# Optimization experiments

Measured on AMD Instinct MI355X. Metric: run time of the kernel, lower is better.

The kernel has to match this reference:

```python
import jax, jax.numpy as jnp
import numpy as np
import math

DIM = 2048
N_HEADS = 32
N_KV_HEADS = 8
HEAD_DIM = DIM // N_HEADS  # 64
N_REP = N_HEADS // N_KV_HEADS  # 4
BSZ, SEQ = 2, 2048


def setup_inputs() -> dict:
    key = jax.random.key(0)
    ks = jax.random.split(key, 8)
    x = jax.random.normal(ks[0], (BSZ, SEQ, DIM), dtype=jnp.float32)
    # rotary tables, [seq, head_dim//2]
    inv_freq = 1.0 / (10000.0 ** (np.arange(0, HEAD_DIM, 2, dtype=np.float32) / HEAD_DIM))
    t = np.arange(SEQ, dtype=np.float32)
    freqs = np.outer(t, inv_freq)
    freqs_cos = jnp.asarray(np.cos(freqs))
    freqs_sin = jnp.asarray(np.sin(freqs))
    s = 0.02
    wq = jax.random.normal(ks[1], (DIM, N_HEADS * HEAD_DIM), dtype=jnp.float32) * s
    wk = jax.random.normal(ks[2], (DIM, N_KV_HEADS * HEAD_DIM), dtype=jnp.float32) * s
    wv = jax.random.normal(ks[3], (DIM, N_KV_HEADS * HEAD_DIM), dtype=jnp.float32) * s
    wo = jax.random.normal(ks[4], (N_HEADS * HEAD_DIM, DIM), dtype=jnp.float32) * s
    return {"x": x, "freqs_cos": freqs_cos, "freqs_sin": freqs_sin,
            "wq": wq, "wk": wk, "wv": wv, "wo": wo}


def _apply_rotary(xq, xk, cos, sin):
    # xq: [b,s,h,d], xk: [b,s,kh,d]; cos/sin: [s, d//2]
    def rot(t):
        tr = t[..., 0::2]  # even -> real
        ti = t[..., 1::2]  # odd  -> imag
        c = cos[None, :, None, :]
        s_ = sin[None, :, None, :]
        or_ = tr * c - ti * s_
        oi_ = tr * s_ + ti * c
        # interleave back: [..., d//2, 2] -> [..., d]
        return jnp.stack([or_, oi_], axis=-1).reshape(t.shape)
    return rot(xq), rot(xk)


def reference(x, freqs_cos, freqs_sin, wq, wk, wv, wo):
    b, s, _ = x.shape
    xq = (x @ wq).reshape(b, s, N_HEADS, HEAD_DIM)
    xk = (x @ wk).reshape(b, s, N_KV_HEADS, HEAD_DIM)
    xv = (x @ wv).reshape(b, s, N_KV_HEADS, HEAD_DIM)
    xq, xk = _apply_rotary(xq, xk, freqs_cos, freqs_sin)
    # repeat_kv: [b,s,kh,d] -> [b,s,kh*n_rep,d]
    xk = jnp.repeat(xk, N_REP, axis=2)
    xv = jnp.repeat(xv, N_REP, axis=2)
    # [b,h,s,d]
    q = xq.transpose(0, 2, 1, 3)
    k = xk.transpose(0, 2, 1, 3)
    v = xv.transpose(0, 2, 1, 3)
    scale = 1.0 / math.sqrt(HEAD_DIM)
    scores = jnp.einsum('bhqd,bhkd->bhqk', q, k) * scale
    causal = jnp.tril(jnp.ones((s, s), dtype=bool))
    scores = jnp.where(causal[None, None], scores, jnp.float32(-jnp.inf))
    probs = jax.nn.softmax(scores, axis=-1)
    out = jnp.einsum('bhqk,bhkd->bhqd', probs, v)  # [b,h,s,d]
    out = out.transpose(0, 2, 1, 3).reshape(b, s, N_HEADS * HEAD_DIM)
    return out @ wo
```

## Files before the change

### kernel.cpp

```cpp
#include <hip/hip_runtime.h>
#include <hip/hip_bf16.h>

typedef __attribute__((ext_vector_type(8))) short short8;
typedef __attribute__((ext_vector_type(4))) float f32x4;

__device__ __forceinline__ unsigned short f2bf(float f) {
  union { float f; unsigned u; } v; v.f = f;
  unsigned r = v.u + 0x7FFFu + ((v.u >> 16) & 1u);
  return (unsigned short)(r >> 16);
}
__device__ __forceinline__ float bf2f(unsigned short h) {
  union { unsigned u; float f; } v; v.u = ((unsigned)h) << 16;
  return v.f;
}
__device__ __forceinline__ unsigned pkbf(float a, float b) {
  __hip_bfloat162 h = __float22bfloat162_rn(float2{a, b});
  union { __hip_bfloat162 h; unsigned u; } cv; cv.h = h;
  return cv.u;
}

__global__ void prep(const float* __restrict__ x, const float* __restrict__ wq,
                     const float* __restrict__ wk, const float* __restrict__ wv,
                     const float* __restrict__ wo, unsigned short* __restrict__ xb,
                     unsigned short* __restrict__ wt, unsigned short* __restrict__ wot) {
  const int z = blockIdx.z, tid = threadIdx.x;
  if (z == 0) {
    int id = blockIdx.y * 64 + blockIdx.x;
#pragma unroll
    for (int rep = 0; rep < 2; ++rep) {
      int i = (rep * 4096 + id) * 256 + tid;
      float4 v = ((const float4*)x)[i];
      ushort4 o;
      o.x = f2bf(v.x); o.y = f2bf(v.y); o.z = f2bf(v.z); o.w = f2bf(v.w);
      ((ushort4*)xb)[i] = o;
    }
    return;
  }
  __shared__ float tile[32][33];
  const float* src;
  unsigned short* dst;
  int N;
  if (z == 1) { src = wq; dst = wt; N = 2048; }
  else if (z == 2) { src = wk; dst = wt + 2048ull * 2048; N = 512; }
  else if (z == 3) { src = wv; dst = wt + 2560ull * 2048; N = 512; }
  else { src = wo; dst = wot; N = 2048; }
  const int K = 2048;
  int n0 = blockIdx.x * 32, k0 = blockIdx.y * 32;
  if (n0 >= N) return;
  int xx = tid & 31, yy = tid >> 5;
#pragma unroll
  for (int j = 0; j < 4; ++j) tile[yy + 8 * j][xx] = src[(size_t)(k0 + yy + 8 * j) * N + n0 + xx];
  __syncthreads();
#pragma unroll
  for (int j = 0; j < 4; ++j) dst[(size_t)(n0 + yy + 8 * j) * K + k0 + xx] = f2bf(tile[xx][yy + 8 * j]);
}

template <int MODE>
__global__ __launch_bounds__(256, 2) void gemm_bt64(const unsigned short* __restrict__ A,
                                                    const unsigned short* __restrict__ Bt,
                                                    void* __restrict__ Cv, int K, int ldc,
                                                    unsigned short* __restrict__ vt,
                                                    const float* __restrict__ fcos,
                                                    const float* __restrict__ fsin) {
  __shared__ alignas(16) unsigned short As[128 * 64];
  __shared__ alignas(16) unsigned short Bs[128 * 64];
  const int t = threadIdx.x;
  const int lane = t & 63, w = t >> 6;
  const int l15 = lane & 15, quad = lane >> 4;
  const int bn0 = blockIdx.x * 128, bm0 = blockIdx.y * 128;
  const int wm = (w >> 1) * 64, wn = (w & 1) * 64;
  const unsigned short* Ab = A + (size_t)bm0 * K;
  const unsigned short* Bb = Bt + (size_t)bn0 * K;
  const int asw = l15 & 7;

  f32x4 acc[4][4];
  const f32x4 zf = {0.f, 0.f, 0.f, 0.f};
#pragma unroll
  for (int i = 0; i < 4; ++i)
#pragma unroll
    for (int j = 0; j < 4; ++j) acc[i][j] = zf;

  for (int k0 = 0; k0 < K; k0 += 64) {
    __syncthreads();
#pragma unroll
    for (int r = 0; r < 4; ++r) {
      int e = r * 256 + t;
      int row = e >> 3, cslot = e & 7;
      int cg = cslot ^ (row & 7);
      const unsigned short* ga = Ab + (size_t)row * K + k0 + cg * 8;
      __builtin_amdgcn_global_load_lds((const __attribute__((address_space(1))) void*)ga,
                                       (__attribute__((address_space(3))) void*)(As + e * 8), 16, 0, 0);
      const unsigned short* gb = Bb + (size_t)row * K + k0 + cg * 8;
      __builtin_amdgcn_global_load_lds((const __attribute__((address_space(1))) void*)gb,
                                       (__attribute__((address_space(3))) void*)(Bs + e * 8), 16, 0, 0);
    }
    __syncthreads();
#pragma unroll
    for (int s = 0; s < 2; ++s) {
      short8 af[4], bf[4];
#pragma unroll
      for (int i = 0; i < 4; ++i)
        af[i] = *reinterpret_cast<const short8*>(As + (wm + i * 16 + l15) * 64 + (((s * 4 + quad) ^ asw) * 8));
#pragma unroll
      for (int j = 0; j < 4; ++j)
        bf[j] = *reinterpret_cast<const short8*>(Bs + (wn + j * 16 + l15) * 64 + (((s * 4 + quad) ^ asw) * 8));
      __builtin_amdgcn_s_setprio(1);
#pragma unroll
      for (int i = 0; i < 4; ++i)
#pragma unroll
        for (int j = 0; j < 4; ++j)
          acc[i][j] = __builtin_amdgcn_mfma_f32_16x16x32_bf16(af[i], bf[j], acc[i][j], 0, 0, 0);
      __builtin_amdgcn_s_setprio(0);
    }
  }

  if (MODE == 1 && bn0 >= 2560) {
    const int b = bm0 >> 11;
#pragma unroll
    for (int i = 0; i < 4; ++i) {
      int srow = (bm0 + wm + i * 16 + quad * 4) & 2047;
#pragma unroll
      for (int j = 0; j < 4; ++j) {
        int vcol = bn0 - 2560 + wn + j * 16 + l15;
        int kvh = vcol >> 6, d = vcol & 63;
        uint2 pk = make_uint2(pkbf(acc[i][j][0], acc[i][j][1]), pkbf(acc[i][j][2], acc[i][j][3]));
        *reinterpret_cast<uint2*>(vt + ((size_t)(b * 8 + kvh) * 64 + d) * 2048 + srow) = pk;
      }
    }
  } else if (MODE == 1 && bn0 >= 2048) {
#pragma unroll
    for (int i = 0; i < 4; ++i)
#pragma unroll
      for (int j = 0; j < 4; ++j)
#pragma unroll
        for (int r = 0; r < 4; ++r) {
          int row = bm0 + wm + i * 16 + quad * 4 + r;
          int s = row & 2047;
          int col = bn0 + wn + j * 16 + l15;
          int fi = ((col - 2048) >> 1) & 31;
          float val = acc[i][j][r];
          float par = __shfl_xor(val, 1, 64);
          float c = fcos[s * 32 + fi], sn = fsin[s * 32 + fi];
          float o = (lane & 1) ? (par * sn + val * c) : (val * c - par * sn);
          ((unsigned short*)Cv)[(size_t)row * ldc + col] = f2bf(o);
        }
  } else {
#pragma unroll
    for (int i = 0; i < 4; ++i)
#pragma unroll
      for (int j = 0; j < 4; ++j)
#pragma unroll
        for (int r = 0; r < 4; ++r) {
          size_t row = (size_t)(bm0 + wm + i * 16 + quad * 4 + r);
          size_t col = (size_t)(bn0 + wn + j * 16 + l15);
          if (MODE == 1)
            ((unsigned short*)Cv)[row * ldc + col] = f2bf(acc[i][j][r]);
          else
            ((float*)Cv)[row * ldc + col] = acc[i][j][r];
        }
  }
}

__global__ __launch_bounds__(256, 4) void flash_attn(const unsigned short* __restrict__ qkv,
                                                     const unsigned short* __restrict__ vt,
                                                     const float* __restrict__ fcos,
                                                     const float* __restrict__ fsin,
                                                     unsigned short* __restrict__ out) {
  __shared__ alignas(16) unsigned short Ks[64 * 64];
  __shared__ alignas(16) unsigned short Vs[64 * 64];
  __shared__ alignas(16) unsigned short Ps[128 * 64];
  const int t = threadIdx.x, lane = t & 63, w = t >> 6;
  const int l15 = lane & 15, quad = lane >> 4;
  const int h = blockIdx.y, b = blockIdx.z;
  const int qb = ((int)blockIdx.x ^ (15 * (h >> 4))) & 15;
  const int q0 = qb * 128;
  const int kvh = h >> 2;
  const size_t rowB = (size_t)b * 2048;
  const unsigned short* Qg = qkv + (rowB + q0) * 2560 + h * 64;
  const unsigned short* Kg = qkv + rowB * 2560 + 2048 + kvh * 64;
  const unsigned short* Vtg = vt + (size_t)(b * 8 + kvh) * 64 * 2048;
  const float SC = 0.18033688011112042f;

  short8 qf[2][2];
#pragma unroll
  for (int mt = 0; mt < 2; ++mt)
#pragma unroll
    for (int s = 0; s < 2; ++s) {
      int qrow = w * 32 + mt * 16 + l15;
      short8 raw = *reinterpret_cast<const short8*>(Qg + (size_t)qrow * 2560 + s * 32 + quad * 8);
      f32x4 c4 = *reinterpret_cast<const f32x4*>(fcos + (size_t)(q0 + qrow) * 32 + s * 16 + quad * 4);
      f32x4 s4 = *reinterpret_cast<const f32x4*>(fsin + (size_t)(q0 + qrow) * 32 + s * 16 + quad * 4);
      short8 o;
#pragma unroll
      for (int k = 0; k < 4; ++k) {
        float xr = bf2f((unsigned short)raw[2 * k]);
        float xi = bf2f((unsigned short)raw[2 * k + 1]);
        o[2 * k] = (short)f2bf((xr * c4[k] - xi * s4[k]) * SC);
        o[2 * k + 1] = (short)f2bf((xr * s4[k] + xi * c4[k]) * SC);
      }
      qf[mt][s] = o;
    }

  const f32x4 zf = {0.f, 0.f, 0.f, 0.f};
  f32x4 oacc[2][4], lacc[2];
#pragma unroll
  for (int mt = 0; mt < 2; ++mt) {
    lacc[mt] = zf;
#pragma unroll
    for (int nt = 0; nt < 4; ++nt) oacc[mt][nt] = zf;
  }
  short8 onesf;
#pragma unroll
  for (int k = 0; k < 8; ++k) onesf[k] = (short)0x3F80;

  const int kb_end = 2 * qb + 2;
  const int srow = t >> 3, sc8 = t & 7;
  const int soff = srow * 64 + ((sc8 ^ (srow & 7)) * 8);
  const int asw = l15 & 7;
  short8 kreg[2], vreg[2];
#pragma unroll
  for (int r = 0; r < 2; ++r) {
    kreg[r] = *reinterpret_cast<const short8*>(Kg + (size_t)(srow + 32 * r) * 2560 + sc8 * 8);
    vreg[r] = *reinterpret_cast<const short8*>(Vtg + (size_t)(srow + 32 * r) * 2048 + sc8 * 8);
  }

  for (int kb = 0; kb < kb_end; ++kb) {
    __syncthreads();
#pragma unroll
    for (int r = 0; r < 2; ++r) {
      *reinterpret_cast<short8*>(Ks + soff + r * 32 * 64) = kreg[r];
      *reinterpret_cast<short8*>(Vs + soff + r * 32 * 64) = vreg[r];
    }
    __syncthreads();
    if (kb + 1 < kb_end) {
#pragma unroll
      for (int r = 0; r < 2; ++r) {
        kreg[r] = *reinterpret_cast<const short8*>(Kg + (size_t)((kb + 1) * 64 + srow + 32 * r) * 2560 + sc8 * 8);
        vreg[r] = *reinterpret_cast<const short8*>(Vtg + (size_t)(srow + 32 * r) * 2048 + (kb + 1) * 64 + sc8 * 8);
      }
    }
    const int qmaxw = q0 + w * 32 + 31;
    if (kb * 64 > qmaxw) continue;
    const bool needMask = (kb * 64 + 63) > (q0 + w * 32);

#pragma unroll
    for (int kvt = 0; kvt < 4; ++kvt) {
      f32x4 st0 = zf, st1 = zf;
#pragma unroll
      for (int s = 0; s < 2; ++s) {
        short8 kf = *reinterpret_cast<const short8*>(Ks + (kvt * 16 + l15) * 64 + ((s * 4 + quad) ^ asw) * 8);
        __builtin_amdgcn_s_setprio(1);
        st0 = __builtin_amdgcn_mfma_f32_16x16x32_bf16(kf, qf[0][s], st0, 0, 0, 0);
        st1 = __builtin_amdgcn_mfma_f32_16x16x32_bf16(kf, qf[1][s], st1, 0, 0, 0);
        __builtin_amdgcn_s_setprio(0);
      }
      const int pcol = ((kvt * 2 + (quad >> 1)) ^ asw) * 8 + (quad & 1) * 4;
      if (needMask) {
        const int kvb = kb * 64 + kvt * 16 + quad * 4;
#pragma unroll
        for (int qt = 0; qt < 2; ++qt) {
          const f32x4 stv = qt ? st1 : st0;
          const int qg = q0 + w * 32 + qt * 16 + l15;
          float p[4];
#pragma unroll
          for (int r = 0; r < 4; ++r) {
            float pv = __builtin_amdgcn_exp2f(stv[r]);
            p[r] = (kvb + r > qg) ? 0.f : pv;
          }
          *reinterpret_cast<uint2*>(Ps + (size_t)(w * 32 + qt * 16 + l15) * 64 + pcol) =
              make_uint2(pkbf(p[0], p[1]), pkbf(p[2], p[3]));
        }
      } else {
#pragma unroll
        for (int qt = 0; qt < 2; ++qt) {
          const f32x4 stv = qt ? st1 : st0;
          float p[4];
#pragma unroll
          for (int r = 0; r < 4; ++r) p[r] = __builtin_amdgcn_exp2f(stv[r]);
          *reinterpret_cast<uint2*>(Ps + (size_t)(w * 32 + qt * 16 + l15) * 64 + pcol) =
              make_uint2(pkbf(p[0], p[1]), pkbf(p[2], p[3]));
        }
      }
    }

#pragma unroll
    for (int s = 0; s < 2; ++s) {
      short8 vf[4];
#pragma unroll
      for (int nt = 0; nt < 4; ++nt)
        vf[nt] = *reinterpret_cast<const short8*>(Vs + (nt * 16 + l15) * 64 + ((s * 4 + quad) ^ asw) * 8);
#pragma unroll
      for (int mt = 0; mt < 2; ++mt) {
        short8 pf = *reinterpret_cast<const short8*>(Ps + (size_t)(w * 32 + mt * 16 + l15) * 64 + ((s * 4 + quad) ^ asw) * 8);
        __builtin_amdgcn_s_setprio(1);
#pragma unroll
        for (int nt = 0; nt < 4; ++nt)
          oacc[mt][nt] = __builtin_amdgcn_mfma_f32_16x16x32_bf16(pf, vf[nt], oacc[mt][nt], 0, 0, 0);
        lacc[mt] = __builtin_amdgcn_mfma_f32_16x16x32_bf16(pf, onesf, lacc[mt], 0, 0, 0);
        __builtin_amdgcn_s_setprio(0);
      }
    }
  }

  float linv[2][4];
#pragma unroll
  for (int mt = 0; mt < 2; ++mt)
#pragma unroll
    for (int r = 0; r < 4; ++r) linv[mt][r] = 1.f / lacc[mt][r];

#pragma unroll
  for (int mt = 0; mt < 2; ++mt)
#pragma unroll
    for (int nt = 0; nt < 4; ++nt)
#pragma unroll
      for (int r = 0; r < 4; ++r) {
        size_t row = rowB + (size_t)(q0 + w * 32 + mt * 16 + quad * 4 + r);
        size_t col = (size_t)h * 64 + nt * 16 + l15;
        out[row * 2048 + col] = f2bf(oacc[mt][nt][r] * linv[mt][r]);
      }
}

extern "C" void kernel_launch(void* const* d_in, const int* in_sizes, int n_in, void* d_out,
                              int out_size, void* d_ws, size_t ws_size, hipStream_t stream) {
  const float* x = (const float*)d_in[0];
  const float* fcos = (const float*)d_in[1];
  const float* fsin = (const float*)d_in[2];
  const float* wq = (const float*)d_in[3];
  const float* wk = (const float*)d_in[4];
  const float* wv = (const float*)d_in[5];
  const float* wo = (const float*)d_in[6];

  char* ws = (char*)d_ws;
  unsigned short* xb = (unsigned short*)ws;
  unsigned short* wt = (unsigned short*)(ws + 16777216ull);
  unsigned short* wot = (unsigned short*)(ws + 29360128ull);
  unsigned short* qkv = (unsigned short*)(ws + 37748736ull);
  unsigned short* attno = (unsigned short*)(ws + 58720256ull);
  unsigned short* vt = (unsigned short*)(ws + 75497472ull);

  prep<<<dim3(64, 64, 5), 256, 0, stream>>>(x, wq, wk, wv, wo, xb, wt, wot);
  gemm_bt64<1><<<dim3(24, 32), 256, 0, stream>>>(xb, wt, qkv, 2048, 2560, vt, fcos, fsin);
  flash_attn<<<dim3(16, 32, 2), 256, 0, stream>>>(qkv, vt, fcos, fsin, attno);
  gemm_bt64<0><<<dim3(16, 32), 256, 0, stream>>>(attno, wot, d_out, 2048, 2048, nullptr, nullptr, nullptr);
}
```

Baseline: 266.3 us.

## Enlarge flash-attention tiles to 256 queries and 128 keys per block

The attention kernel now uses 512-thread blocks covering 256 query rows, and stages 128-key K/V tiles per barrier, processed as two 64-key halves. This halves the grid, amortises K/V global loads across more warps, and halves the number of barrier-separated stage iterations. The causal tile ordering is changed to an XOR by batch to balance load. In exchange, shared memory and per-block register demand grow, which may reduce occupancy, and the larger causal blocks give coarser load imbalance.

Result: slower. 292.9 us (+10.0%).

```diff
diff --git a/kernel.cpp b/kernel.cpp
--- a/kernel.cpp
+++ b/kernel.cpp
@@ -161,19 +161,19 @@
   }
 }
 
-__global__ __launch_bounds__(256, 4) void flash_attn(const unsigned short* __restrict__ qkv,
+__global__ __launch_bounds__(512, 4) void flash_attn(const unsigned short* __restrict__ qkv,
                                                      const unsigned short* __restrict__ vt,
                                                      const float* __restrict__ fcos,
                                                      const float* __restrict__ fsin,
                                                      unsigned short* __restrict__ out) {
-  __shared__ alignas(16) unsigned short Ks[64 * 64];
-  __shared__ alignas(16) unsigned short Vs[64 * 64];
-  __shared__ alignas(16) unsigned short Ps[128 * 64];
+  __shared__ alignas(16) unsigned short Ks[128 * 64];
+  __shared__ alignas(16) unsigned short Vs[64 * 128];
+  __shared__ alignas(16) unsigned short Ps[256 * 64];
   const int t = threadIdx.x, lane = t & 63, w = t >> 6;
   const int l15 = lane & 15, quad = lane >> 4;
   const int h = blockIdx.y, b = blockIdx.z;
-  const int qb = ((int)blockIdx.x ^ (15 * (h >> 4))) & 15;
-  const int q0 = qb * 128;
+  const int qb = (int)blockIdx.x ^ (b ? 7 : 0);
+  const int q0 = qb * 256;
   const int kvh = h >> 2;
   const size_t rowB = (size_t)b * 2048;
   const unsigned short* Qg = qkv + (rowB + q0) * 2560 + h * 64;
@@ -214,90 +214,98 @@
   for (int k = 0; k < 8; ++k) onesf[k] = (short)0x3F80;
 
   const int kb_end = 2 * qb + 2;
-  const int srow = t >> 3, sc8 = t & 7;
-  const int soff = srow * 64 + ((sc8 ^ (srow & 7)) * 8);
+  const int krow0 = t >> 3, kc = t & 7;
+  const int vrow0 = t >> 4, vc = t & 15;
+  const int soffK = krow0 * 64 + ((kc ^ (krow0 & 7)) * 8);
+  const int soffV = vrow0 * 128 + ((vc ^ (vrow0 & 7)) * 8);
   const int asw = l15 & 7;
   short8 kreg[2], vreg[2];
 #pragma unroll
   for (int r = 0; r < 2; ++r) {
-    kreg[r] = *reinterpret_cast<const short8*>(Kg + (size_t)(srow + 32 * r) * 2560 + sc8 * 8);
-    vreg[r] = *reinterpret_cast<const short8*>(Vtg + (size_t)(srow + 32 * r) * 2048 + sc8 * 8);
-  }
+    kreg[r] = *reinterpret_cast<const short8*>(Kg + (size_t)(krow0 + 64 * r) * 2560 + kc * 8);
+    vreg[r] = *reinterpret_cast<const short8*>(Vtg + (size_t)(vrow0 + 32 * r) * 2048 + vc * 8);
+  }
+
+  const int qmaxw = q0 + w * 32 + 31;
 
   for (int kb = 0; kb < kb_end; ++kb) {
     __syncthreads();
-#pragma unroll
-    for (int r = 0; r < 2; ++r) {
-      *reinterpret_cast<short8*>(Ks + soff + r * 32 * 64) = kreg[r];
-      *reinterpret_cast<short8*>(Vs + soff + r * 32 * 64) = vreg[r];
-    }
+    *reinterpret_cast<short8*>(Ks + soffK) = kreg[0];
+    *reinterpret_cast<short8*>(Ks + soffK + 64 * 64) = kreg[1];
+    *reinterpret_cast<short8*>(Vs + soffV) = vreg[0];
+    *reinterpret_cast<short8*>(Vs + soffV + 32 * 128) = vreg[1];
     __syncthreads();
     if (kb + 1 < kb_end) {
 #pragma unroll
       for (int r = 0; r < 2; ++r) {
-        kreg[r] = *reinterpret_cast<const short8*>(Kg + (size_t)((kb + 1) * 64 + srow + 32 * r) * 2560 + sc8 * 8);
-        vreg[r] = *reinterpret_cast<const short8*>(Vtg + (size_t)(srow + 32 * r) * 2048 + (kb + 1) * 64 + sc8 * 8);
-      }
-    }
-    const int qmaxw = q0 + w * 32 + 31;
-    if (kb * 64 > qmaxw) continue;
-    const bool needMask = (kb * 64 + 63) > (q0 + w * 32);
-
-#pragma unroll
-    for (int kvt = 0; kvt < 4; ++kvt) {
-      f32x4 st0 = zf, st1 = zf;
+        kreg[r] = *reinterpret_cast<const short8*>(Kg + (size_t)((kb + 1) * 128 + krow0 + 64 * r) * 2560 + kc * 8);
+        vreg[r] = *reinterpret_cast<const short8*>(Vtg + (size_t)(vrow0 + 32 * r) * 2048 + (kb + 1) * 128 + vc * 8);
+      }
+    }
+    if (kb * 128 > qmaxw) continue;
+
+#pragma unroll
+    for (int hf = 0; hf < 2; ++hf) {
+      const int base = kb * 128 + hf * 64;
+      if (base > qmaxw) break;
+      const bool needMask = (base + 63) > (q0 + w * 32);
+
+#pragma unroll
+      for (int kvt = 0; kvt < 4; ++kvt) {
+        f32x4 st0 = zf, st1 = zf;
+#pragma unroll
+        for (int s = 0; s < 2; ++s) {
+          short8 kf = *reinterpret_cast<const short8*>(Ks + (hf * 64 + kvt * 16 + l15) * 64 + ((s * 4 + quad) ^ asw) * 8);
+          __builtin_amdgcn_s_setprio(1);
+          st0 = __builtin_amdgcn_mfma_f32_16x16x32_bf16(kf, qf[0][s], st0, 0, 0, 0);
+          st1 = __builtin_amdgcn_mfma_f32_16x16x32_bf16(kf, qf[1][s], st1, 0, 0, 0);
+          __builtin_amdgcn_s_setprio(0);
+        }
+        const int pcol = ((kvt * 2 + (quad >> 1)) ^ asw) * 8 + (quad & 1) * 4;
+        if (needMask) {
+          const int kvb = base + kvt * 16 + quad * 4;
+#pragma unroll
+          for (int qt = 0; qt < 2; ++qt) {
+            const f32x4 stv = qt ? st1 : st0;
+            const int qg = q0 + w * 32 + qt * 16 + l15;
+            float p[4];
+#pragma unroll
+            for (int r = 0; r < 4; ++r) {
+              float pv = __builtin_amdgcn_exp2f(stv[r]);
+              p[r] = (kvb + r > qg) ? 0.f : pv;
+            }
+            *reinterpret_cast<uint2*>(Ps + (size_t)(w * 32 + qt * 16 + l15) * 64 + pcol) =
+                make_uint2(pkbf(p[0], p[1]), pkbf(p[2], p[3]));
+          }
+        } else {
+#pragma unroll
+          for (int qt = 0; qt < 2; ++qt) {
+            const f32x4 stv = qt ? st1 : st0;
+            float p[4];
+#pragma unroll
+            for (int r = 0; r < 4; ++r) p[r] = __builtin_amdgcn_exp2f(stv[r]);
+            *reinterpret_cast<uint2*>(Ps + (size_t)(w * 32 + qt * 16 + l15) * 64 + pcol) =
+                make_uint2(pkbf(p[0], p[1]), pkbf(p[2], p[3]));
+          }
+        }
+      }
+
 #pragma unroll
       for (int s = 0; s < 2; ++s) {
-        short8 kf = *reinterpret_cast<const short8*>(Ks + (kvt * 16 + l15) * 64 + ((s * 4 + quad) ^ asw) * 8);
-        __builtin_amdgcn_s_setprio(1);
-        st0 = __builtin_amdgcn_mfma_f32_16x16x32_bf16(kf, qf[0][s], st0, 0, 0, 0);
-        st1 = __builtin_amdgcn_mfma_f32_16x16x32_bf16(kf, qf[1][s], st1, 0, 0, 0);
-        __builtin_amdgcn_s_setprio(0);
-      }
-      const int pcol = ((kvt * 2 + (quad >> 1)) ^ asw) * 8 + (quad & 1) * 4;
-      if (needMask) {
-        const int kvb = kb * 64 + kvt * 16 + quad * 4;
-#pragma unroll
-        for (int qt = 0; qt < 2; ++qt) {
-          const f32x4 stv = qt ? st1 : st0;
-          const int qg = q0 + w * 32 + qt * 16 + l15;
-          float p[4];
-#pragma unroll
-          for (int r = 0; r < 4; ++r) {
-            float pv = __builtin_amdgcn_exp2f(stv[r]);
-            p[r] = (kvb + r > qg) ? 0.f : pv;
-          }
-          *reinterpret_cast<uint2*>(Ps + (size_t)(w * 32 + qt * 16 + l15) * 64 + pcol) =
-              make_uint2(pkbf(p[0], p[1]), pkbf(p[2], p[3]));
-        }
-      } else {
-#pragma unroll
-        for (int qt = 0; qt < 2; ++qt) {
-          const f32x4 stv = qt ? st1 : st0;
-          float p[4];
-#pragma unroll
-          for (int r = 0; r < 4; ++r) p[r] = __builtin_amdgcn_exp2f(stv[r]);
-          *reinterpret_cast<uint2*>(Ps + (size_t)(w * 32 + qt * 16 + l15) * 64 + pcol) =
-              make_uint2(pkbf(p[0], p[1]), pkbf(p[2], p[3]));
-        }
-      }
-    }
-
-#pragma unroll
-    for (int s = 0; s < 2; ++s) {
-      short8 vf[4];
-#pragma unroll
-      for (int nt = 0; nt < 4; ++nt)
-        vf[nt] = *reinterpret_cast<const short8*>(Vs + (nt * 16 + l15) * 64 + ((s * 4 + quad) ^ asw) * 8);
-#pragma unroll
-      for (int mt = 0; mt < 2; ++mt) {
-        short8 pf = *reinterpret_cast<const short8*>(Ps + (size_t)(w * 32 + mt * 16 + l15) * 64 + ((s * 4 + quad) ^ asw) * 8);
-        __builtin_amdgcn_s_setprio(1);
+        short8 vf[4];
 #pragma unroll
         for (int nt = 0; nt < 4; ++nt)
-          oacc[mt][nt] = __builtin_amdgcn_mfma_f32_16x16x32_bf16(pf, vf[nt], oacc[mt][nt], 0, 0, 0);
-        lacc[mt] = __builtin_amdgcn_mfma_f32_16x16x32_bf16(pf, onesf, lacc[mt], 0, 0, 0);
-        __builtin_amdgcn_s_setprio(0);
+          vf[nt] = *reinterpret_cast<const short8*>(Vs + (nt * 16 + l15) * 128 + (((hf * 2 + s) * 4 + quad) ^ asw) * 8);
+#pragma unroll
+        for (int mt = 0; mt < 2; ++mt) {
+          short8 pf = *reinterpret_cast<const short8*>(Ps + (size_t)(w * 32 + mt * 16 + l15) * 64 + ((s * 4 + quad) ^ asw) * 8);
+          __builtin_amdgcn_s_setprio(1);
+#pragma unroll
+          for (int nt = 0; nt < 4; ++nt)
+            oacc[mt][nt] = __builtin_amdgcn_mfma_f32_16x16x32_bf16(pf, vf[nt], oacc[mt][nt], 0, 0, 0);
+          lacc[mt] = __builtin_amdgcn_mfma_f32_16x16x32_bf16(pf, onesf, lacc[mt], 0, 0, 0);
+          __builtin_amdgcn_s_setprio(0);
+        }
       }
     }
   }
@@ -340,6 +348,6 @@
 
   prep<<<dim3(64, 64, 5), 256, 0, stream>>>(x, wq, wk, wv, wo, xb, wt, wot);
   gemm_bt64<1><<<dim3(24, 32), 256, 0, stream>>>(xb, wt, qkv, 2048, 2560, vt, fcos, fsin);
-  flash_attn<<<dim3(16, 32, 2), 256, 0, stream>>>(qkv, vt, fcos, fsin, attno);
+  flash_attn<<<dim3(8, 32, 2), 512, 0, stream>>>(qkv, vt, fcos, fsin, attno);
   gemm_bt64<0><<<dim3(16, 32), 256, 0, stream>>>(attno, wot, d_out, 2048, 2048, nullptr, nullptr, nullptr);
 }
```
